# Performance work log

Hardware: AMD Instinct MI355X
Metric: run time of the kernel (lower is better)

Reference implementation:

```python
import jax, jax.numpy as jnp
import numpy as np

HEADS = 12
BUCKETS = 256          # position_buckets -> pos_ebd_size (att_span)
MAXPOS = 512           # max_relative_positions
GAMMA = 0.0            # forward() default gamma
LN_EPS = 1e-7


def _make_log_bucket_position(rel, bucket_size, max_position):
    # numpy, host-side constant (shapes are static)
    mid = bucket_size // 2
    sign = np.sign(rel)
    abs_pos = np.where((rel < mid) & (rel > -mid), mid - 1, np.abs(rel)).astype(np.float32)
    log_pos = np.ceil(np.log(abs_pos / mid) / np.log((max_position - 1) / mid) * (mid - 1)) + mid
    return np.where(abs_pos <= mid, rel, (log_pos * sign).astype(np.int64)).astype(np.int64)


def _build_relative_position(q_size, k_size):
    rel = np.arange(q_size)[:, None] - np.arange(k_size)[None, :]
    return _make_log_bucket_position(rel, BUCKETS, MAXPOS)  # [q, k] int64


def _pproc_linear(x, W, b, gamma):
    # pproc: zp * stop_grad(z / zp) with player weights = W + gamma*relu(W)
    z = x @ W.T + b
    pW = W + gamma * jnp.clip(W, 0.0, None)
    pb = b + gamma * jnp.clip(b, 0.0, None)
    zp = x @ pW.T + pb
    return zp * jax.lax.stop_gradient(z / zp)


def setup_inputs() -> dict:
    key = jax.random.key(0)
    ks = jax.random.split(key, 12)
    B, S, H = 4, 1024, 768
    s = 0.02
    return {
        "hidden_states": jax.random.normal(ks[0], (B, S, H), jnp.float32),
        "rel_embeddings": jax.random.normal(ks[1], (2 * BUCKETS, H), jnp.float32),
        "Wq": jax.random.normal(ks[2], (H, H), jnp.float32) * s,
        "bq": jax.random.normal(ks[3], (H,), jnp.float32) * s,
        "Wk": jax.random.normal(ks[4], (H, H), jnp.float32) * s,
        "bk": jax.random.normal(ks[5], (H,), jnp.float32) * s,
        "Wv": jax.random.normal(ks[6], (H, H), jnp.float32) * s,
        "bv": jax.random.normal(ks[7], (H,), jnp.float32) * s,
        "Wo": jax.random.normal(ks[8], (H, H), jnp.float32) * s,
        "bo": jax.random.normal(ks[9], (H,), jnp.float32) * s,
        "ln_w": jnp.ones((H,), jnp.float32),
        "ln_b": jnp.zeros((H,), jnp.float32),
    }


def reference(hidden_states, rel_embeddings, Wq, bq, Wk, bk, Wv, bv, Wo, bo, ln_w, ln_b):
    B, S, H = hidden_states.shape
    d = H // HEADS
    span = BUCKETS  # att_span = pos_ebd_size

    # Q/K/V via pproc dual-layer trick (eval mode, gamma=0 -> plain linear fwd)
    q = _pproc_linear(hidden_states, Wq, bq, GAMMA).reshape(B, S, HEADS, d).transpose(0, 2, 1, 3)
    k = _pproc_linear(hidden_states, Wk, bk, GAMMA).reshape(B, S, HEADS, d).transpose(0, 2, 1, 3)
    v = _pproc_linear(hidden_states, Wv, bv, GAMMA).reshape(B, S, HEADS, d).transpose(0, 2, 1, 3)

    scale_factor = 3.0  # 1 + c2p + p2c
    scale = jnp.sqrt(jnp.float32(d) * scale_factor)
    scores = jnp.einsum("bhsd,bhtd->bhst", q, k) / scale  # [B,H,S,S]

    # disentangled attention bias
    rel = jnp.asarray(_build_relative_position(S, S))  # [S,S] int64 bucketed
    pos_emb = rel_embeddings[: 2 * span]               # [2K, H]
    # share_att_key=True: reuse query/key projections (plain, no pproc)
    pos_k = (pos_emb @ Wk.T + bk).reshape(2 * span, HEADS, d).transpose(1, 0, 2)  # [H,2K,d]
    pos_q = (pos_emb @ Wq.T + bq).reshape(2 * span, HEADS, d).transpose(1, 0, 2)  # [H,2K,d]

    # c2p: gather over bucket axis
    c2p_att = jnp.einsum("bhsd,hkd->bhsk", q, pos_k)                      # [B,H,S,2K]
    c2p_idx = jnp.clip(rel + span, 0, 2 * span - 1)[None, None]           # [1,1,S,S]
    c2p = jnp.take_along_axis(c2p_att, jnp.broadcast_to(c2p_idx, (B, HEADS, S, S)), axis=-1) / scale

    # p2c: gather then transpose
    p2c_att = jnp.einsum("bhtd,hkd->bhtk", k, pos_q)                      # [B,H,S,2K]
    p2c_idx = jnp.clip(-rel + span, 0, 2 * span - 1)[None, None]
    p2c = jnp.take_along_axis(p2c_att, jnp.broadcast_to(p2c_idx, (B, HEADS, S, S)), axis=-1)
    p2c = jnp.swapaxes(p2c, -1, -2) / scale

    scores = scores + c2p + p2c
    probs = jax.lax.stop_gradient(jax.nn.softmax(scores, axis=-1))  # .detach() in original

    ctx = jnp.einsum("bhst,bhtd->bhsd", probs, v).transpose(0, 2, 1, 3).reshape(B, S, H)

    # self_output.pforward: pproc dense + residual + LayerNorm
    out = _pproc_linear(ctx, Wo, bo, GAMMA) + hidden_states
    mu = jnp.mean(out, axis=-1, keepdims=True)
    var = jnp.mean(jnp.square(out - mu), axis=-1, keepdims=True)
    out = ln_w * (out - mu) / jnp.sqrt(var + LN_EPS) + ln_b
    return out, probs
```

## Files before the change

kernel.cpp:

```cpp
#include <hip/hip_runtime.h>

#define BB 4
#define SS 1024
#define HH 768
#define NH 12
#define DD 64
#define SPAN 256
#define TWOSPAN 512
#define NBH (BB * NH)
#define TOT (BB * SS * HH)
#define POSTOT (TWOSPAN * HH)
#define WTOT (HH * HH)
#define QKVLD 2304

typedef unsigned short u16;
typedef __attribute__((ext_vector_type(8))) short bf16x8;
typedef __attribute__((ext_vector_type(4))) float f32x4;

__device__ u16 g_hid[TOT];
__device__ u16 g_rel[POSTOT];
__device__ u16 g_W3[3 * WTOT];
__device__ u16 g_b3[3 * HH];
__device__ u16 g_Wo[WTOT];
__device__ u16 g_bo[HH];
__device__ u16 g_lnw[HH];
__device__ u16 g_lnb[HH];

__device__ u16 g_qkv[(BB * SS) * QKVLD];
__device__ u16 g_posqk[TWOSPAN * 1536];
__device__ u16 g_ctx[TOT];

__device__ u16 g_vt[NBH * DD * SS];
__device__ u16 g_c2p[48 * 1024 * 512];
__device__ u16 g_p2cT[48 * 512 * 1024];
__device__ float g_oproj[TOT];
__device__ int g_relidx[2048];
__device__ int g_isfp32;

__device__ __forceinline__ float b2f(u16 u) {
    union { unsigned int i; float f; } x;
    x.i = ((unsigned int)u) << 16;
    return x.f;
}
__device__ __forceinline__ u16 f2b(float f) {
    union { float f; unsigned int i; } x;
    x.f = f;
    unsigned int r = x.i + 0x7fffu + ((x.i >> 16) & 1u);
    return (u16)(r >> 16);
}

typedef const __attribute__((address_space(1))) unsigned int gas_uint;
typedef __attribute__((address_space(3))) unsigned int las_uint;
__device__ __forceinline__ void gl2lds16(const u16* gp, u16* lp) {
    __builtin_amdgcn_global_load_lds((gas_uint*)gp, (las_uint*)lp, 16, 0, 0);
}

__global__ void detect_dtype(const u16* __restrict__ hid) {
    __shared__ int cnt;
    if (threadIdx.x == 0) cnt = 0;
    __syncthreads();
    const u16 u = hid[threadIdx.x * 2];
    const int e = (u >> 7) & 0xFF;
    if (e >= 130) atomicAdd(&cnt, 1);
    __syncthreads();
    if (threadIdx.x == 0) g_isfp32 = (cnt >= 16) ? 1 : 0;
}

struct Srcs { const void* p[12]; };
#define NCVT (TOT + POSTOT + 4 * WTOT + 6 * HH + 2047)

__device__ __forceinline__ u16 cvt1(const void* p, long long i, int isf) {
    return isf ? f2b(((const float*)p)[i]) : ((const u16*)p)[i];
}

__global__ void fused_convert(Srcs s) {
    long long r = (long long)blockIdx.x * 256 + threadIdx.x;
    const int isf = g_isfp32;
    if (r < TOT) { g_hid[r] = cvt1(s.p[0], r, isf); return; }  r -= TOT;
    if (r < POSTOT) { g_rel[r] = cvt1(s.p[1], r, isf); return; }  r -= POSTOT;
    if (r < WTOT) { g_W3[r] = cvt1(s.p[2], r, isf); return; }  r -= WTOT;
    if (r < WTOT) { g_W3[WTOT + r] = cvt1(s.p[4], r, isf); return; }  r -= WTOT;
    if (r < WTOT) { g_W3[2 * WTOT + r] = cvt1(s.p[6], r, isf); return; }  r -= WTOT;
    if (r < WTOT) { g_Wo[r] = cvt1(s.p[8], r, isf); return; }  r -= WTOT;
    if (r < HH) { g_b3[r] = cvt1(s.p[3], r, isf); return; }  r -= HH;
    if (r < HH) { g_b3[HH + r] = cvt1(s.p[5], r, isf); return; }  r -= HH;
    if (r < HH) { g_b3[2 * HH + r] = cvt1(s.p[7], r, isf); return; }  r -= HH;
    if (r < HH) { g_bo[r] = cvt1(s.p[9], r, isf); return; }  r -= HH;
    if (r < HH) { g_lnw[r] = cvt1(s.p[10], r, isf); return; }  r -= HH;
    if (r < HH) { g_lnb[r] = cvt1(s.p[11], r, isf); return; }  r -= HH;
    if (r < 2047) {
        int delta = (int)r - 1023;
        int ad = delta < 0 ? -delta : delta;
        int bucket;
        if (ad <= 128) {
            bucket = delta;
        } else {
            float num = logf((float)ad / 128.0f);
            double v = (double)num / log(511.0 / 128.0) * 127.0;
            int lp = (int)ceil(v) + 128;
            bucket = (delta > 0) ? lp : -lp;
        }
        int idx = bucket + SPAN;
        idx = idx < 0 ? 0 : (idx > 511 ? 511 : idx);
        g_relidx[r] = idx;
    }
}

__global__ __launch_bounds__(256) void mfma_nt_gemm(
    const u16* __restrict__ A, const u16* __restrict__ B, const u16* __restrict__ bias,
    void* __restrict__ C, int lda, int ldb, int ldc, int K, int c_f32,
    unsigned long long aSb, unsigned long long aSh,
    unsigned long long bSb, unsigned long long bSh,
    unsigned long long cSb, unsigned long long cSh)
{
    const int z = blockIdx.z;
    const int bz = z / NH, hz = z % NH;
    A += (size_t)bz * aSb + (size_t)hz * aSh;
    B += (size_t)bz * bSb + (size_t)hz * bSh;
    const size_t coff = (size_t)bz * cSb + (size_t)hz * cSh;

    __shared__ u16 As[128 * 64];
    __shared__ u16 Bs[128 * 64];

    const int tid = threadIdx.x;
    const int w  = tid >> 6;
    const int l  = tid & 63;
    const int lr = l & 15;
    const int hi = l >> 4;
    const int rr = hi << 2;
    const int m0 = blockIdx.y * 128;
    const int n0 = blockIdx.x * 128;
    const int wm = (w >> 1) * 64;
    const int wn = (w & 1) * 64;
    const int srow = l >> 3;
    const int scol = (l & 7) * 8;

    f32x4 acc[4][4] = {};
    for (int k0 = 0; k0 < K; k0 += 64) {
        #pragma unroll
        for (int ii = 0; ii < 4; ++ii) {
            const int ch = w * 4 + ii;
            const int r  = ch * 8 + srow;
            gl2lds16(A + (size_t)(m0 + r) * lda + k0 + scol, &As[ch * 512]);
            gl2lds16(B + (size_t)(n0 + r) * ldb + k0 + scol, &Bs[ch * 512]);
        }
        __syncthreads();

        #pragma unroll
        for (int kk = 0; kk < 2; ++kk) {
            bf16x8 af[4], bfr[4];
            #pragma unroll
            for (int m = 0; m < 4; ++m)
                af[m] = *(const bf16x8*)&As[(wm + m * 16 + lr) * 64 + kk * 32 + hi * 8];
            #pragma unroll
            for (int n = 0; n < 4; ++n)
                bfr[n] = *(const bf16x8*)&Bs[(wn + n * 16 + lr) * 64 + kk * 32 + hi * 8];
            #pragma unroll
            for (int m = 0; m < 4; ++m)
                #pragma unroll
                for (int n = 0; n < 4; ++n)
                    acc[m][n] = __builtin_amdgcn_mfma_f32_16x16x32_bf16(af[m], bfr[n], acc[m][n], 0, 0, 0);
        }
        __syncthreads();
    }

    #pragma unroll
    for (int m = 0; m < 4; ++m) {
        #pragma unroll
        for (int n = 0; n < 4; ++n) {
            const int col = n0 + wn + n * 16 + lr;
            const float bv = bias ? b2f(bias[col]) : 0.f;
            #pragma unroll
            for (int r = 0; r < 4; ++r) {
                const int row = m0 + wm + m * 16 + rr + r;
                const float v = acc[m][n][r] + bv;
                if (c_f32) ((float*)C)[coff + (size_t)row * ldc + col] = v;
                else       ((u16*)C)[coff + (size_t)row * ldc + col]  = f2b(v);
            }
        }
    }
}

__global__ void vtrans_kernel() {
    const int i = blockIdx.x * 256 + threadIdx.x;
    const int d = i & 63;
    const int t = (i >> 6) & 1023;
    const int z = i >> 16;
    const int b = z / NH, h = z % NH;
    g_vt[((size_t)z * DD + d) * SS + t] =
        g_qkv[((size_t)(b * SS + t)) * QKVLD + 2 * HH + h * DD + d];
}

__global__ __launch_bounds__(256, 3) void attn_fused_kernel(void* __restrict__ dout, int has_probs)
{
    const int nblk = blockIdx.x;
    const int xcd  = nblk & 7;
    const int jj0  = nblk >> 3;
    const int z    = xcd * 6 + (jj0 >> 6);
    const int s0   = (jj0 & 63) * 16;
    const int b    = z / NH, h = z % NH;
    const int tid  = threadIdx.x;
    const int w    = tid >> 6;
    const int l    = tid & 63;
    const int lr   = l & 15;
    const int hi   = l >> 4;
    const int lk8  = hi << 3;
    const int rr   = hi << 2;

    __shared__ __align__(16) char smem[32768];
    __shared__ int   relw[1040];
    __shared__ float redm[4][16];
    __shared__ float reds[4][16];

    for (int i = tid; i < 1040; i += 256) relw[i] = g_relidx[s0 + i];

    const u16* __restrict__ qb = g_qkv + ((size_t)(b * SS + s0)) * QKVLD + h * DD;
    const u16* __restrict__ kb = g_qkv + ((size_t)(b * SS)) * QKVLD + HH + h * DD;
    const bf16x8 aq0 = *(const bf16x8*)(qb + (size_t)lr * QKVLD + lk8);
    const bf16x8 aq1 = *(const bf16x8*)(qb + (size_t)lr * QKVLD + 32 + lk8);

    const int t0 = w * 256;
    f32x4 acc[16];
    #pragma unroll
    for (int nn = 0; nn < 16; ++nn) {
        const u16* kp = kb + (size_t)(t0 + nn * 16 + lr) * QKVLD;
        const bf16x8 bk0 = *(const bf16x8*)(kp + lk8);
        const bf16x8 bk1 = *(const bf16x8*)(kp + 32 + lk8);
        f32x4 a = {};
        a = __builtin_amdgcn_mfma_f32_16x16x32_bf16(aq0, bk0, a, 0, 0, 0);
        a = __builtin_amdgcn_mfma_f32_16x16x32_bf16(aq1, bk1, a, 0, 0, 0);
        acc[nn] = a;
    }
    __syncthreads();

    const float rscale = 0.07216878364870323f;
    const u16* __restrict__ c2pb = g_c2p  + ((size_t)z * SS + s0) * TWOSPAN;
    const u16* __restrict__ p2cb = g_p2cT + (size_t)z * TWOSPAN * SS;
    #pragma unroll
    for (int nn = 0; nn < 16; ++nn) {
        const int t = t0 + nn * 16 + lr;
        #pragma unroll
        for (int r = 0; r < 4; ++r) {
            const int srow = rr + r;
            const int j = relw[srow - t + 1023];
            acc[nn][r] = (acc[nn][r] + b2f(c2pb[srow * TWOSPAN + j])
                                     + b2f(p2cb[(size_t)j * SS + t])) * rscale;
        }
    }

    float mr[4];
    #pragma unroll
    for (int r = 0; r < 4; ++r) {
        float m = acc[0][r];
        #pragma unroll
        for (int nn = 1; nn < 16; ++nn) m = fmaxf(m, acc[nn][r]);
        #pragma unroll
        for (int off = 1; off < 16; off <<= 1) m = fmaxf(m, __shfl_xor(m, off));
        mr[r] = m;
    }
    if (lr == 0) {
        #pragma unroll
        for (int r = 0; r < 4; ++r) redm[w][rr + r] = mr[r];
    }
    __syncthreads();
    #pragma unroll
    for (int r = 0; r < 4; ++r) {
        const int srow = rr + r;
        mr[r] = fmaxf(fmaxf(redm[0][srow], redm[1][srow]),
                      fmaxf(redm[2][srow], redm[3][srow]));
    }

    float sr[4] = {0.f, 0.f, 0.f, 0.f};
    #pragma unroll
    for (int nn = 0; nn < 16; ++nn)
        #pragma unroll
        for (int r = 0; r < 4; ++r) {
            const float e = __expf(acc[nn][r] - mr[r]);
            acc[nn][r] = e;
            sr[r] += e;
        }
    #pragma unroll
    for (int r = 0; r < 4; ++r)
        #pragma unroll
        for (int off = 1; off < 16; off <<= 1) sr[r] += __shfl_xor(sr[r], off);
    if (lr == 0) {
        #pragma unroll
        for (int r = 0; r < 4; ++r) reds[w][rr + r] = sr[r];
    }
    __syncthreads();
    float inv[4];
    #pragma unroll
    for (int r = 0; r < 4; ++r) {
        const int srow = rr + r;
        inv[r] = 1.0f / (reds[0][srow] + reds[1][srow] + reds[2][srow] + reds[3][srow]);
    }

    const int isf = g_isfp32;
    #pragma unroll
    for (int nn = 0; nn < 16; ++nn) {
        const int t = t0 + nn * 16 + lr;
        #pragma unroll
        for (int r = 0; r < 4; ++r) {
            const int srow = rr + r;
            const float pv = acc[nn][r] * inv[r];
            const u16 pb = f2b(pv);
            *(u16*)(smem + (srow * 2048 + ((((t >> 3) ^ (srow & 7)) << 4) | ((t & 7) << 1)))) = pb;
            if (has_probs) {
                const size_t base = (size_t)TOT + ((size_t)z * SS + (s0 + srow)) * SS + t;
                if (isf) ((float*)dout)[base] = pv;
                else     ((u16*)dout)[base]   = pb;
            }
        }
    }
    __syncthreads();

    const u16* __restrict__ VT = g_vt + (size_t)z * DD * SS;
    f32x4 cacc[4] = {};
    #pragma unroll
    for (int ks = 0; ks < 8; ++ks) {
        const int kt = t0 + ks * 32;
        const int tA = kt + lk8;
        const bf16x8 pa = *(const bf16x8*)(smem + (lr * 2048 + ((((tA >> 3) ^ (lr & 7)) << 4))));
        #pragma unroll
        for (int nn = 0; nn < 4; ++nn) {
            const bf16x8 bv = *(const bf16x8*)(VT + (size_t)(nn * 16 + lr) * SS + kt + lk8);
            cacc[nn] = __builtin_amdgcn_mfma_f32_16x16x32_bf16(pa, bv, cacc[nn], 0, 0, 0);
        }
    }
    __syncthreads();

    float* ctxp = (float*)smem;
    #pragma unroll
    for (int nn = 0; nn < 4; ++nn)
        #pragma unroll
        for (int r = 0; r < 4; ++r) {
            const int srow = rr + r;
            const int d = nn * 16 + lr;
            ctxp[w * 1024 + srow * 64 + (d ^ ((srow & 3) << 4))] = cacc[nn][r];
        }
    __syncthreads();

    #pragma unroll
    for (int it = 0; it < 4; ++it) {
        const int idx = it * 256 + tid;
        const int srow = idx >> 6;
        const int d = idx & 63;
        const int dd = d ^ ((srow & 3) << 4);
        const float rsum = ctxp[srow * 64 + dd] + ctxp[1024 + srow * 64 + dd]
                         + ctxp[2048 + srow * 64 + dd] + ctxp[3072 + srow * 64 + dd];
        g_ctx[((size_t)(b * SS + s0 + srow)) * HH + h * DD + d] = f2b(rsum);
    }
}

__global__ __launch_bounds__(256) void ln_kernel(void* __restrict__ dout)
{
    const int row = blockIdx.x;
    const int tid = threadIdx.x;
    __shared__ float os[HH];
    __shared__ float red[4];

    for (int c = tid; c < HH; c += 256)
        os[c] = g_oproj[(size_t)row * HH + c] + b2f(g_hid[(size_t)row * HH + c]);
    __syncthreads();

    float sum = 0.f;
    for (int c = tid; c < HH; c += 256) sum += os[c];
    #pragma unroll
    for (int off = 32; off > 0; off >>= 1) sum += __shfl_down(sum, off);
    if ((tid & 63) == 0) red[tid >> 6] = sum;
    __syncthreads();
    if (tid == 0) red[0] = red[0] + red[1] + red[2] + red[3];
    __syncthreads();
    const float mu = red[0] * (1.0f / HH);
    __syncthreads();

    float vs = 0.f;
    for (int c = tid; c < HH; c += 256) {
        const float dd0 = os[c] - mu;
        vs += dd0 * dd0;
    }
    #pragma unroll
    for (int off = 32; off > 0; off >>= 1) vs += __shfl_down(vs, off);
    if ((tid & 63) == 0) red[tid >> 6] = vs;
    __syncthreads();
    if (tid == 0) red[0] = red[0] + red[1] + red[2] + red[3];
    __syncthreads();
    const float var = red[0] * (1.0f / HH);
    const float rstd = 1.0f / sqrtf(var + 1e-7f);

    const int isf = g_isfp32;
    for (int c = tid; c < HH; c += 256) {
        const float o = b2f(g_lnw[c]) * (os[c] - mu) * rstd + b2f(g_lnb[c]);
        if (isf) ((float*)dout)[(size_t)row * HH + c] = o;
        else     ((u16*)dout)[(size_t)row * HH + c]   = f2b(o);
    }
}

extern "C" void kernel_launch(void* const* d_in, const int* in_sizes, int n_in,
                              void* d_out, int out_size, void* d_ws, size_t ws_size,
                              hipStream_t stream) {
    detect_dtype<<<1, 256, 0, stream>>>((const u16*)d_in[0]);

    Srcs s;
    for (int i = 0; i < 12; ++i) s.p[i] = d_in[i];
    fused_convert<<<(NCVT + 255) / 256, 256, 0, stream>>>(s);

    void* p;
    u16 *p_hid, *p_rel, *p_W3, *p_b3, *p_Wo, *p_bo, *p_qkv, *p_posqk, *p_ctx;
    u16 *p_c2p, *p_p2cT;
    float *p_oproj;
    (void)hipGetSymbolAddress(&p, HIP_SYMBOL(g_hid));   p_hid   = (u16*)p;
    (void)hipGetSymbolAddress(&p, HIP_SYMBOL(g_rel));   p_rel   = (u16*)p;
    (void)hipGetSymbolAddress(&p, HIP_SYMBOL(g_W3));    p_W3    = (u16*)p;
    (void)hipGetSymbolAddress(&p, HIP_SYMBOL(g_b3));    p_b3    = (u16*)p;
    (void)hipGetSymbolAddress(&p, HIP_SYMBOL(g_Wo));    p_Wo    = (u16*)p;
    (void)hipGetSymbolAddress(&p, HIP_SYMBOL(g_bo));    p_bo    = (u16*)p;
    (void)hipGetSymbolAddress(&p, HIP_SYMBOL(g_qkv));   p_qkv   = (u16*)p;
    (void)hipGetSymbolAddress(&p, HIP_SYMBOL(g_posqk)); p_posqk = (u16*)p;
    (void)hipGetSymbolAddress(&p, HIP_SYMBOL(g_ctx));   p_ctx   = (u16*)p;
    (void)hipGetSymbolAddress(&p, HIP_SYMBOL(g_c2p));   p_c2p   = (u16*)p;
    (void)hipGetSymbolAddress(&p, HIP_SYMBOL(g_p2cT));  p_p2cT  = (u16*)p;
    (void)hipGetSymbolAddress(&p, HIP_SYMBOL(g_oproj)); p_oproj = (float*)p;

    const int M = BB * SS;
    const unsigned long long Z = 0ull;

    mfma_nt_gemm<<<dim3(QKVLD / 128, M / 128, 1), 256, 0, stream>>>(
        p_hid, p_W3, p_b3, p_qkv, HH, HH, QKVLD, HH, 0, Z, Z, Z, Z, Z, Z);
    mfma_nt_gemm<<<dim3(1536 / 128, TWOSPAN / 128, 1), 256, 0, stream>>>(
        p_rel, p_W3, p_b3, p_posqk, HH, HH, 1536, HH, 0, Z, Z, Z, Z, Z, Z);

    mfma_nt_gemm<<<dim3(TWOSPAN / 128, SS / 128, NBH), 256, 0, stream>>>(
        p_qkv, p_posqk + HH, (const u16*)nullptr, p_c2p, QKVLD, 1536, TWOSPAN, DD, 0,
        (unsigned long long)SS * QKVLD, (unsigned long long)DD,
        Z,                              (unsigned long long)DD,
        (unsigned long long)NH * SS * TWOSPAN, (unsigned long long)SS * TWOSPAN);
    mfma_nt_gemm<<<dim3(SS / 128, TWOSPAN / 128, NBH), 256, 0, stream>>>(
        p_posqk, p_qkv + HH, (const u16*)nullptr, p_p2cT, 1536, QKVLD, SS, DD, 0,
        Z,                               (unsigned long long)DD,
        (unsigned long long)SS * QKVLD,  (unsigned long long)DD,
        (unsigned long long)NH * TWOSPAN * SS, (unsigned long long)TWOSPAN * SS);

    vtrans_kernel<<<(NBH * DD * SS) / 256, 256, 0, stream>>>();

    const long long need = (long long)TOT + (long long)BB * NH * SS * SS;
    const int has_probs = ((long long)out_size >= need) ? 1 : 0;
    attn_fused_kernel<<<NBH * (SS / 16), 256, 0, stream>>>(d_out, has_probs);

    mfma_nt_gemm<<<dim3(HH / 128, M / 128, 1), 256, 0, stream>>>(
        p_ctx, p_Wo, p_bo, p_oproj, HH, HH, HH, HH, 1, Z, Z, Z, Z, Z, Z);

    ln_kernel<<<BB * SS, 256, 0, stream>>>(d_out);
}
```

Baseline: 623.4 us.

## Stage c2p in LDS, store p2c row-major, vectorize probs and convert

The p2c GEMM now writes [t][j] row-major instead of the transposed layout, so the per-key gather reads within one row rather than striding by SS. The c2p tile for the block's 16 rows is loaded into LDS with global_load_lds before the QK MFMAs, replacing scattered global gathers. Probability output moves from scalar per-element stores inside the register loop to vectorized 16-byte stores read back from the swizzled LDS tile. The input conversion handles 8 elements per thread with vector loads, and launch bounds go from 3 to 4 waves, which may raise register pressure or cause spills.

```diff
diff --git a/kernel.cpp b/kernel.cpp
--- a/kernel.cpp
+++ b/kernel.cpp
@@ -17,22 +17,22 @@
 typedef __attribute__((ext_vector_type(8))) short bf16x8;
 typedef __attribute__((ext_vector_type(4))) float f32x4;
 
-__device__ u16 g_hid[TOT];
-__device__ u16 g_rel[POSTOT];
-__device__ u16 g_W3[3 * WTOT];
-__device__ u16 g_b3[3 * HH];
-__device__ u16 g_Wo[WTOT];
-__device__ u16 g_bo[HH];
-__device__ u16 g_lnw[HH];
-__device__ u16 g_lnb[HH];
-
-__device__ u16 g_qkv[(BB * SS) * QKVLD];
-__device__ u16 g_posqk[TWOSPAN * 1536];
-__device__ u16 g_ctx[TOT];
-
-__device__ u16 g_vt[NBH * DD * SS];
-__device__ u16 g_c2p[48 * 1024 * 512];
-__device__ u16 g_p2cT[48 * 512 * 1024];
+__device__ __align__(16) u16 g_hid[TOT];
+__device__ __align__(16) u16 g_rel[POSTOT];
+__device__ __align__(16) u16 g_W3[3 * WTOT];
+__device__ __align__(16) u16 g_b3[3 * HH];
+__device__ __align__(16) u16 g_Wo[WTOT];
+__device__ __align__(16) u16 g_bo[HH];
+__device__ __align__(16) u16 g_lnw[HH];
+__device__ __align__(16) u16 g_lnb[HH];
+
+__device__ __align__(16) u16 g_qkv[(BB * SS) * QKVLD];
+__device__ __align__(16) u16 g_posqk[TWOSPAN * 1536];
+__device__ __align__(16) u16 g_ctx[TOT];
+
+__device__ __align__(16) u16 g_vt[NBH * DD * SS];
+__device__ __align__(16) u16 g_c2p[48 * 1024 * 512];
+__device__ __align__(16) u16 g_p2c[48 * 1024 * 512];
 __device__ float g_oproj[TOT];
 __device__ int g_relidx[2048];
 __device__ int g_isfp32;
@@ -67,27 +67,40 @@
 }
 
 struct Srcs { const void* p[12]; };
-#define NCVT (TOT + POSTOT + 4 * WTOT + 6 * HH + 2047)
-
-__device__ __forceinline__ u16 cvt1(const void* p, long long i, int isf) {
-    return isf ? f2b(((const float*)p)[i]) : ((const u16*)p)[i];
+#define NCVT8 ((TOT + POSTOT + 4 * WTOT + 6 * HH) / 8)
+
+__device__ __forceinline__ void cvt8(const void* sp, long long off, u16* dp, int isf) {
+    if (isf) {
+        const float* f = (const float*)sp + off;
+        const float4 a = *(const float4*)f;
+        const float4 b = *(const float4*)(f + 4);
+        u16 o[8] = { f2b(a.x), f2b(a.y), f2b(a.z), f2b(a.w),
+                     f2b(b.x), f2b(b.y), f2b(b.z), f2b(b.w) };
+        *(bf16x8*)(dp + off) = *(const bf16x8*)o;
+    } else {
+        *(bf16x8*)(dp + off) = *(const bf16x8*)((const u16*)sp + off);
+    }
 }
 
 __global__ void fused_convert(Srcs s) {
-    long long r = (long long)blockIdx.x * 256 + threadIdx.x;
+    const long long i = (long long)blockIdx.x * 256 + threadIdx.x;
     const int isf = g_isfp32;
-    if (r < TOT) { g_hid[r] = cvt1(s.p[0], r, isf); return; }  r -= TOT;
-    if (r < POSTOT) { g_rel[r] = cvt1(s.p[1], r, isf); return; }  r -= POSTOT;
-    if (r < WTOT) { g_W3[r] = cvt1(s.p[2], r, isf); return; }  r -= WTOT;
-    if (r < WTOT) { g_W3[WTOT + r] = cvt1(s.p[4], r, isf); return; }  r -= WTOT;
-    if (r < WTOT) { g_W3[2 * WTOT + r] = cvt1(s.p[6], r, isf); return; }  r -= WTOT;
-    if (r < WTOT) { g_Wo[r] = cvt1(s.p[8], r, isf); return; }  r -= WTOT;
-    if (r < HH) { g_b3[r] = cvt1(s.p[3], r, isf); return; }  r -= HH;
-    if (r < HH) { g_b3[HH + r] = cvt1(s.p[5], r, isf); return; }  r -= HH;
-    if (r < HH) { g_b3[2 * HH + r] = cvt1(s.p[7], r, isf); return; }  r -= HH;
-    if (r < HH) { g_bo[r] = cvt1(s.p[9], r, isf); return; }  r -= HH;
-    if (r < HH) { g_lnw[r] = cvt1(s.p[10], r, isf); return; }  r -= HH;
-    if (r < HH) { g_lnb[r] = cvt1(s.p[11], r, isf); return; }  r -= HH;
+    if (i < NCVT8) {
+        long long r = i * 8;
+        if (r < TOT) { cvt8(s.p[0], r, g_hid, isf); return; }  r -= TOT;
+        if (r < POSTOT) { cvt8(s.p[1], r, g_rel, isf); return; }  r -= POSTOT;
+        if (r < WTOT) { cvt8(s.p[2], r, g_W3, isf); return; }  r -= WTOT;
+        if (r < WTOT) { cvt8(s.p[4], r, g_W3 + WTOT, isf); return; }  r -= WTOT;
+        if (r < WTOT) { cvt8(s.p[6], r, g_W3 + 2 * WTOT, isf); return; }  r -= WTOT;
+        if (r < WTOT) { cvt8(s.p[8], r, g_Wo, isf); return; }  r -= WTOT;
+        if (r < HH) { cvt8(s.p[3], r, g_b3, isf); return; }  r -= HH;
+        if (r < HH) { cvt8(s.p[5], r, g_b3 + HH, isf); return; }  r -= HH;
+        if (r < HH) { cvt8(s.p[7], r, g_b3 + 2 * HH, isf); return; }  r -= HH;
+        if (r < HH) { cvt8(s.p[9], r, g_bo, isf); return; }  r -= HH;
+        if (r < HH) { cvt8(s.p[10], r, g_lnw, isf); return; }  r -= HH;
+        cvt8(s.p[11], r, g_lnb, isf); return;
+    }
+    const long long r = i - NCVT8;
     if (r < 2047) {
         int delta = (int)r - 1023;
         int ad = delta < 0 ? -delta : delta;
@@ -191,7 +204,7 @@
         g_qkv[((size_t)(b * SS + t)) * QKVLD + 2 * HH + h * DD + d];
 }
 
-__global__ __launch_bounds__(256, 3) void attn_fused_kernel(void* __restrict__ dout, int has_probs)
+__global__ __launch_bounds__(256, 4) void attn_fused_kernel(void* __restrict__ dout, int has_probs)
 {
     const int nblk = blockIdx.x;
     const int xcd  = nblk & 7;
@@ -214,6 +227,16 @@
 
     for (int i = tid; i < 1040; i += 256) relw[i] = g_relidx[s0 + i];
 
+    u16* c2p_lds = (u16*)smem;
+    {
+        const u16* __restrict__ c2pg = g_c2p + ((size_t)z * SS + s0) * TWOSPAN;
+        #pragma unroll
+        for (int ii = 0; ii < 4; ++ii) {
+            const int row = w * 4 + ii;
+            gl2lds16(c2pg + (size_t)row * TWOSPAN + l * 8, &c2p_lds[row * 520]);
+        }
+    }
+
     const u16* __restrict__ qb = g_qkv + ((size_t)(b * SS + s0)) * QKVLD + h * DD;
     const u16* __restrict__ kb = g_qkv + ((size_t)(b * SS)) * QKVLD + HH + h * DD;
     const bf16x8 aq0 = *(const bf16x8*)(qb + (size_t)lr * QKVLD + lk8);
@@ -234,17 +257,17 @@
     __syncthreads();
 
     const float rscale = 0.07216878364870323f;
-    const u16* __restrict__ c2pb = g_c2p  + ((size_t)z * SS + s0) * TWOSPAN;
-    const u16* __restrict__ p2cb = g_p2cT + (size_t)z * TWOSPAN * SS;
+    const u16* __restrict__ p2cb = g_p2c + (size_t)z * SS * TWOSPAN;
     #pragma unroll
     for (int nn = 0; nn < 16; ++nn) {
         const int t = t0 + nn * 16 + lr;
+        const u16* __restrict__ p2crow = p2cb + (size_t)t * TWOSPAN;
         #pragma unroll
         for (int r = 0; r < 4; ++r) {
             const int srow = rr + r;
             const int j = relw[srow - t + 1023];
-            acc[nn][r] = (acc[nn][r] + b2f(c2pb[srow * TWOSPAN + j])
-                                     + b2f(p2cb[(size_t)j * SS + t])) * rscale;
+            acc[nn][r] = (acc[nn][r] + b2f(c2p_lds[srow * 520 + j])
+                                     + b2f(p2crow[j])) * rscale;
         }
     }
 
@@ -295,7 +318,6 @@
         inv[r] = 1.0f / (reds[0][srow] + reds[1][srow] + reds[2][srow] + reds[3][srow]);
     }
 
-    const int isf = g_isfp32;
     #pragma unroll
     for (int nn = 0; nn < 16; ++nn) {
         const int t = t0 + nn * 16 + lr;
@@ -303,16 +325,34 @@
         for (int r = 0; r < 4; ++r) {
             const int srow = rr + r;
             const float pv = acc[nn][r] * inv[r];
-            const u16 pb = f2b(pv);
-            *(u16*)(smem + (srow * 2048 + ((((t >> 3) ^ (srow & 7)) << 4) | ((t & 7) << 1)))) = pb;
-            if (has_probs) {
-                const size_t base = (size_t)TOT + ((size_t)z * SS + (s0 + srow)) * SS + t;
-                if (isf) ((float*)dout)[base] = pv;
-                else     ((u16*)dout)[base]   = pb;
+            *(u16*)(smem + (srow * 2048 + ((((t >> 3) ^ (srow & 7)) << 4) | ((t & 7) << 1)))) = f2b(pv);
+        }
+    }
+    __syncthreads();
+
+    const int isf = g_isfp32;
+    if (has_probs) {
+        const int prow = tid >> 4;
+        const int pc0  = tid & 15;
+        const int swz  = prow & 7;
+        const size_t gbase = (size_t)TOT + ((size_t)z * SS + (s0 + prow)) * SS;
+        #pragma unroll
+        for (int k = 0; k < 8; ++k) {
+            const int tc = pc0 + k * 16;
+            const bf16x8 pv8 = *(const bf16x8*)(smem + prow * 2048 + ((tc ^ swz) << 4));
+            if (isf) {
+                float4 f0, f1;
+                f0.x = b2f((u16)pv8[0]); f0.y = b2f((u16)pv8[1]);
+                f0.z = b2f((u16)pv8[2]); f0.w = b2f((u16)pv8[3]);
+                f1.x = b2f((u16)pv8[4]); f1.y = b2f((u16)pv8[5]);
+                f1.z = b2f((u16)pv8[6]); f1.w = b2f((u16)pv8[7]);
+                *(float4*)((float*)dout + gbase + (size_t)tc * 8)     = f0;
+                *(float4*)((float*)dout + gbase + (size_t)tc * 8 + 4) = f1;
+            } else {
+                *(bf16x8*)((u16*)dout + gbase + (size_t)tc * 8) = pv8;
             }
         }
     }
-    __syncthreads();
 
     const u16* __restrict__ VT = g_vt + (size_t)z * DD * SS;
     f32x4 cacc[4] = {};
@@ -403,11 +443,11 @@
 
     Srcs s;
     for (int i = 0; i < 12; ++i) s.p[i] = d_in[i];
-    fused_convert<<<(NCVT + 255) / 256, 256, 0, stream>>>(s);
+    fused_convert<<<(int)((NCVT8 + 2047 + 255) / 256), 256, 0, stream>>>(s);
 
     void* p;
     u16 *p_hid, *p_rel, *p_W3, *p_b3, *p_Wo, *p_bo, *p_qkv, *p_posqk, *p_ctx;
-    u16 *p_c2p, *p_p2cT;
+    u16 *p_c2p, *p_p2c;
     float *p_oproj;
     (void)hipGetSymbolAddress(&p, HIP_SYMBOL(g_hid));   p_hid   = (u16*)p;
     (void)hipGetSymbolAddress(&p, HIP_SYMBOL(g_rel));   p_rel   = (u16*)p;
@@ -419,7 +459,7 @@
     (void)hipGetSymbolAddress(&p, HIP_SYMBOL(g_posqk)); p_posqk = (u16*)p;
     (void)hipGetSymbolAddress(&p, HIP_SYMBOL(g_ctx));   p_ctx   = (u16*)p;
     (void)hipGetSymbolAddress(&p, HIP_SYMBOL(g_c2p));   p_c2p   = (u16*)p;
-    (void)hipGetSymbolAddress(&p, HIP_SYMBOL(g_p2cT));  p_p2cT  = (u16*)p;
+    (void)hipGetSymbolAddress(&p, HIP_SYMBOL(g_p2c));   p_p2c   = (u16*)p;
     (void)hipGetSymbolAddress(&p, HIP_SYMBOL(g_oproj)); p_oproj = (float*)p;
 
     const int M = BB * SS;
@@ -435,11 +475,11 @@
         (unsigned long long)SS * QKVLD, (unsigned long long)DD,
         Z,                              (unsigned long long)DD,
         (unsigned long long)NH * SS * TWOSPAN, (unsigned long long)SS * TWOSPAN);
-    mfma_nt_gemm<<<dim3(SS / 128, TWOSPAN / 128, NBH), 256, 0, stream>>>(
-        p_posqk, p_qkv + HH, (const u16*)nullptr, p_p2cT, 1536, QKVLD, SS, DD, 0,
-        Z,                               (unsigned long long)DD,
-        (unsigned long long)SS * QKVLD,  (unsigned long long)DD,
-        (unsigned long long)NH * TWOSPAN * SS, (unsigned long long)TWOSPAN * SS);
+    mfma_nt_gemm<<<dim3(TWOSPAN / 128, SS / 128, NBH), 256, 0, stream>>>(
+        p_qkv + HH, p_posqk, (const u16*)nullptr, p_p2c, QKVLD, 1536, TWOSPAN, DD, 0,
+        (unsigned long long)SS * QKVLD, (unsigned long long)DD,
+        Z,                              (unsigned long long)DD,
+        (unsigned long long)NH * SS * TWOSPAN, (unsigned long long)SS * TWOSPAN);
 
     vtrans_kernel<<<(NBH * DD * SS) / 256, 256, 0, stream>>>();
 
```

Result: no change. 611.2 us (-2.0%).
